# Optimization experiments

Measured on AMD Instinct MI355X. Metric: run time of the kernel, lower is better.

## Reference

```python
import jax, jax.numpy as jnp
import numpy as np

H = W = 64
ALPHA = 1.0
BETA = 100.0
LIMB_PAIRS = np.array([[0,1],[1,2],[2,3],[0,4],[4,5],[5,6],[0,7],[7,8],[8,9],[9,10],
                       [8,11],[11,12],[12,13],[8,14],[14,15],[15,16]])
P0 = LIMB_PAIRS[:, 0]
P1 = LIMB_PAIRS[:, 1]
_last = {}
for _l, _j in enumerate(P0):
    _last[int(_j)] = _l
J0 = np.array(list(_last.keys()))   # unique proximal joints
L0 = np.array(list(_last.values())) # last limb writing to each joint


def make_kernel(h, w, alpha):
    # replicates: coords = stack(meshgrid(arange(2h-1), arange(2w-1))).transpose(1,2) (h==w)
    ii, jj = jnp.meshgrid(jnp.arange(2 * h - 1), jnp.arange(2 * w - 1), indexing='ij')
    ker = jnp.stack([h - jj, w - ii], axis=0).astype(jnp.float32)  # (2, 2h-1, 2w-1)
    dist = jnp.linalg.norm(ker, axis=0, keepdims=True)
    dist = dist.at[0, h, w].set(1.0)
    return ker / dist ** (1.0 + alpha)


def corr_full(x, k):
    # x: (N, Cin, h, w); k: (Cout, Cin, 2h-1, 2w-1); 'same' correlation with pad h-1/w-1
    h, w = x.shape[-2:]
    return jax.lax.conv_general_dilated(x, k, (1, 1), ((h - 1, h - 1), (w - 1, w - 1)))


def heatmap_std(x, di=False):
    axes = (3, 4, 5) if di else (3, 4)
    return jnp.std(x, axis=axes, keepdims=True, ddof=1)


def heatmap_normalize(x, std, di=False):
    return x * std / (heatmap_std(x, di) + 1e-6)


def l2norm(v, axis):
    return v / jnp.maximum(jnp.linalg.norm(v, axis=axis, keepdims=True), 1e-12)


def soft_argmax(hm, beta):
    # hm: ... x h x w -> ... x 2 with (row_coord, col_coord) as in the torch code
    h, w = hm.shape[-2:]
    p = jax.nn.softmax(hm.reshape(hm.shape[:-2] + (-1,)) * beta, axis=-1).reshape(hm.shape)
    rows = jnp.arange(h, dtype=p.dtype)[:, None]
    cols = jnp.arange(w, dtype=p.dtype)[None, :]
    norm = p.sum((-2, -1))
    kp_x = (p * rows).sum((-2, -1)) / norm
    kp_y = (p * cols).sum((-2, -1)) / norm
    return jnp.stack((kp_x, kp_y), axis=-1)


def scale_pts(pts, image_shape, h, w):
    return jnp.stack((pts[..., 0] * image_shape[1] / w,
                      pts[..., 1] * image_shape[0] / h), axis=-1)


def cofix_forward(heatmaps, fields, Ps, Rs, Cs, image_shape, confs, vth1, vth2, pth1, pth2):
    bs, nv, nL, _, h, w = fields.shape
    nJ = heatmaps.shape[2]
    K = make_kernel(h, w, ALPHA)  # (2, 2h-1, 2w-1)

    heatmaps = heatmaps - jnp.mean(heatmaps, axis=(3, 4), keepdims=True)
    std_hm = heatmap_std(heatmaps, di=False)
    std_df = heatmap_std(fields, di=True)

    Hs = heatmaps[:, :, P1] - heatmaps[:, :, P0]  # (bs, nv, nL, h, w)
    # conv3d(kernel1, flipped Hs) == 'same' correlation of Hs with spatially-reversed K
    k1 = K[:, ::-1, ::-1][:, None]  # (2, 1, 2h-1, 2w-1)
    convs = corr_full(Hs.reshape(-1, 1, h, w), k1).reshape(bs, nv, nL, 2, h, w)

    coef = jax.nn.relu(jnp.sum(convs * fields[..., :2, :, :], axis=3, keepdims=True))
    fields_new = fields * coef

    fnorm = jnp.linalg.norm(fields, axis=3, keepdims=True)
    lvecs = l2norm(jnp.sum(fnorm * fields, axis=(4, 5)), axis=3)
    lpts = scale_pts(soft_argmax(fnorm[:, :, :, 0], BETA), image_shape, h, w)

    fnorm_new = jnp.linalg.norm(fields_new, axis=3, keepdims=True)
    lvecs_new = l2norm(jnp.sum(fnorm_new * fields_new, axis=(4, 5)), axis=3)
    lpts_new = scale_pts(soft_argmax(fnorm_new[:, :, :, 0], BETA), image_shape, h, w)

    # original code computes vec_selection(...) then overwrites: delta[:] = 0
    delta = jnp.zeros((bs, nv, nL, 1), dtype=heatmaps.dtype)
    comb_v = delta * lvecs_new + (1 - delta) * lvecs
    comb_p = delta * lpts_new + (1 - delta) * lpts

    d6 = delta[..., None, None]
    fields_c = heatmap_normalize(fields * (1 - d6) + fields_new * d6, std_df, di=True)

    # conv2d(kernel2, fields) then output spatial flip == 'same' correlation with K
    k2 = K[None]  # (1, 2, 2h-1, 2w-1)
    fds2jts = corr_full(fields_c[..., :2, :, :].reshape(-1, 2, h, w), k2)
    fds2jts = fds2jts.reshape(bs, nv, nL, h, w)
    prox_ = jax.nn.relu(-fds2jts)
    dist_ = jax.nn.relu(fds2jts)

    hms_new = heatmaps.at[:, :, J0].set(heatmaps[:, :, J0] * prox_[:, :, L0])
    hms_new = hms_new.at[:, :, P1].set(hms_new[:, :, P1] * dist_)
    hms_new = heatmap_normalize(hms_new, std_hm, di=False)

    kps = scale_pts(soft_argmax(heatmaps, BETA), image_shape, h, w)[..., None]
    kps_new = scale_pts(soft_argmax(hms_new, BETA), image_shape, h, w)[..., None]
    kps_new = jnp.where(jnp.isnan(kps_new), kps, kps_new)

    # sed_selection (reconstructed): keep refined kps where joint conf is high and
    # the refinement displacement is small.
    confs_j = confs[:, :, nL:]
    disp = jnp.linalg.norm((kps_new - kps)[..., 0], axis=-1)  # (bs, nv, nJ)
    sel = ((confs_j > pth1) & (disp < pth2)).astype(kps.dtype)[..., None, None]
    kps_combined = sel * kps_new + (1 - sel) * kps

    return kps_combined, comb_v, comb_p, fields_new, hms_new


def setup_inputs() -> dict:
    key = jax.random.key(0)
    ks = jax.random.split(key, 6)
    bs, nv, nJ, nL = 4, 4, 17, 16
    return {
        'heatmaps': jax.random.uniform(ks[0], (bs, nv, nJ, H, W), jnp.float32),
        'fields': jax.random.normal(ks[1], (bs, nv, nL, 3, H, W), jnp.float32),
        'Ps': jax.random.normal(ks[2], (bs, nv, 3, 4), jnp.float32),
        'Rs': jax.random.normal(ks[3], (bs, nv, 3, 3), jnp.float32),
        'Cs': jax.random.normal(ks[4], (bs, nv, 3, 1), jnp.float32),
        'image_shape': jnp.array([384, 384], jnp.int32),
        'confs': jax.random.uniform(ks[5], (bs, nv, nL + nJ), jnp.float32),
        'vth1': 0.5, 'vth2': 0.5, 'pth1': 0.1, 'pth2': 20.0,
    }


def reference(heatmaps, fields, Ps, Rs, Cs, image_shape, confs, vth1, vth2, pth1, pth2):
    return cofix_forward(heatmaps, fields, Ps, Rs, Cs, image_shape, confs,
                         vth1, vth2, pth1, pth2)
```

## Files before the change

### kernel.cpp

```cpp
#include <hip/hip_runtime.h>
#include <math.h>

#define TPB 1024
#define HTPB 256
#define NPIX 4096
#define NJ 17
#define NL 16
static constexpr float kBeta = 100.0f;
static constexpr float S2H = 0.70710678118654752f;

#define O_KPS 0
#define O_CV 544
#define O_CP 1312
#define O_FN 1824
#define O_HM 3147552
#define W_FDS 0
#define W_MEAN 1048576
#define W_STD 1048848
#define W_SF 1049120
#define W_W1 1049376
#define W_W2 1082144

__device__ __constant__ int c_P0[16] = {0,1,2,0,4,5,0,7,8,9,8,11,12,8,14,15};
__device__ __constant__ int c_P1[16] = {1,2,3,4,5,6,7,8,9,10,11,12,13,14,15,16};
__device__ __constant__ int c_proxL[17] = {6,1,2,-1,4,5,-1,7,13,9,-1,11,12,-1,14,15,-1};
__device__ __constant__ int c_distL[17] = {-1,0,1,2,3,4,5,6,7,8,9,10,11,12,13,14,15};

using cplx = float2;
__device__ inline cplx cadd(cplx a, cplx b){ return {a.x+b.x, a.y+b.y}; }
__device__ inline cplx csub(cplx a, cplx b){ return {a.x-b.x, a.y-b.y}; }
__device__ inline cplx cmul(cplx a, cplx w){ return {a.x*w.x - a.y*w.y, a.x*w.y + a.y*w.x}; }
__device__ inline cplx cmulc(cplx a, cplx w){ return {a.x*w.x + a.y*w.y, a.y*w.x - a.x*w.y}; }

__device__ __constant__ float2 W128BR[8] = {
  {1.f,0.f},
  {0.98078528040323044913f,-0.19509032201612826785f},
  {0.99518472667219688624f,-0.09801714032956060199f},
  {0.95694033573220886494f,-0.29028467725446236764f},
  {0.99879545620517239271f,-0.04906767432741801425f},
  {0.97003125319454399260f,-0.24298017990326388995f},
  {0.98917650996478097345f,-0.14673047445536175166f},
  {0.94154406518302077841f,-0.33688985339222005069f}
};
__device__ __constant__ float2 W16BR[8] = {
  {1.f,0.f},
  {0.f,-1.f},
  {0.70710678118654752440f,-0.70710678118654752440f},
  {-0.70710678118654752440f,-0.70710678118654752440f},
  {0.92387953251128675613f,-0.38268343236508977173f},
  {-0.38268343236508977173f,-0.92387953251128675613f},
  {0.38268343236508977173f,-0.92387953251128675613f},
  {-0.92387953251128675613f,-0.38268343236508977173f}
};

__device__ inline void bf8_tail(cplx t0, cplx t1, cplx t2, cplx t3,
                                cplx t4, cplx t5, cplx t6, cplx t7, cplx x[8]){
  cplx u0=cadd(t0,t2), u2=csub(t0,t2);
  cplx u1=cadd(t1,t3), d13=csub(t1,t3);
  cplx u3={d13.y,-d13.x};
  cplx u4=cadd(t4,t6), u6=csub(t4,t6);
  cplx u5=cadd(t5,t7), d57=csub(t5,t7);
  cplx u7={d57.y,-d57.x};
  x[0]=cadd(u0,u1); x[1]=csub(u0,u1);
  x[2]=cadd(u2,u3); x[3]=csub(u2,u3);
  x[4]=cadd(u4,u5); x[5]=csub(u4,u5);
  x[6]=cadd(u6,u7); x[7]=csub(u6,u7);
}
__device__ inline void bf8_fwd(cplx x[8]){
  cplx t0=cadd(x[0],x[4]), d4=csub(x[0],x[4]);
  cplx t1=cadd(x[1],x[5]), d5=csub(x[1],x[5]);
  cplx t2=cadd(x[2],x[6]), d6=csub(x[2],x[6]);
  cplx t3=cadd(x[3],x[7]), d7=csub(x[3],x[7]);
  cplx t5={S2H*(d5.x+d5.y), S2H*(d5.y-d5.x)};
  cplx t6={d6.y,-d6.x};
  cplx t7={S2H*(d7.y-d7.x), -S2H*(d7.x+d7.y)};
  bf8_tail(t0,t1,t2,t3,d4,t5,t6,t7,x);
}
__device__ inline void bf8_fwd_z(cplx x[8]){
  cplx t5={S2H*(x[1].x+x[1].y), S2H*(x[1].y-x[1].x)};
  cplx t6={x[2].y,-x[2].x};
  cplx t7={S2H*(x[3].y-x[3].x), -S2H*(x[3].x+x[3].y)};
  bf8_tail(x[0],x[1],x[2],x[3],x[0],t5,t6,t7,x);
}
__device__ inline void bf8_inv(cplx y[8]){
  cplx u0=cadd(y[0],y[1]), u1=csub(y[0],y[1]);
  cplx u2=cadd(y[2],y[3]), u3=csub(y[2],y[3]);
  cplx u4=cadd(y[4],y[5]), u5=csub(y[4],y[5]);
  cplx u6=cadd(y[6],y[7]), u7=csub(y[6],y[7]);
  cplx t0=cadd(u0,u2), t2=csub(u0,u2);
  cplx iu3={-u3.y,u3.x};
  cplx t1=cadd(u1,iu3), t3=csub(u1,iu3);
  cplx t4=cadd(u4,u6), t6=csub(u4,u6);
  cplx iu7={-u7.y,u7.x};
  cplx t5=cadd(u5,iu7), t7=csub(u5,iu7);
  y[0]=cadd(t0,t4); y[4]=csub(t0,t4);
  cplx w5={S2H*(t5.x-t5.y), S2H*(t5.x+t5.y)};
  y[1]=cadd(t1,w5); y[5]=csub(t1,w5);
  cplx w6={-t6.y,t6.x};
  y[2]=cadd(t2,w6); y[6]=csub(t2,w6);
  cplx w7={-S2H*(t7.x+t7.y), S2H*(t7.x-t7.y)};
  y[3]=cadd(t3,w7); y[7]=csub(t3,w7);
}

__device__ inline void fft16_fwd(cplx z[16]){
  cplx e[8], o[8];
  #pragma unroll
  for (int t=0;t<8;t++){ e[t]=z[2*t]; o[t]=z[2*t+1]; }
  bf8_fwd(e); bf8_fwd(o);
  #pragma unroll
  for (int p=0;p<8;p++){
    cplx vo = cmul(o[p], W16BR[p]);
    z[2*p]   = cadd(e[p], vo);
    z[2*p+1] = csub(e[p], vo);
  }
}
__device__ inline void fft16_inv(cplx z[16]){
  cplx e[8], o[8];
  #pragma unroll
  for (int p=0;p<8;p++){
    cplx a=z[2*p], b=z[2*p+1];
    e[p] = cadd(a,b);
    o[p] = cmulc(csub(a,b), W16BR[p]);
  }
  bf8_inv(e); bf8_inv(o);
  #pragma unroll
  for (int t=0;t<8;t++){ z[2*t]=e[t]; z[2*t+1]=o[t]; }
}

__device__ inline void twchainA(const cplx* TW, int j, cplx A[8]){
  cplx W1 = TW[j];
  cplx W2 = cmul(W1,W1);
  cplx W4 = cmul(W2,W2);
  cplx W6 = cmul(W4,W2);
  A[0] = {1.f,0.f}; A[1] = W4; A[2] = W2; A[3] = W6;
  A[4] = W1; A[5] = cmul(W4,W1); A[6] = cmul(W2,W1); A[7] = cmul(W6,W1);
}

__device__ inline int PH(int y, int m){ return (y<<6) | ((m ^ ((y&7)*9)) & 63); }

template<int NLINES, bool ZT>
__device__ void row_s1_fwd(float4* S4, const cplx* TW, int tid){
  if (tid < NLINES*8){
    const int L = tid>>3, m = tid&7;
    cplx xe[8], xo[8];
    #pragma unroll
    for (int t=0; t<(ZT?4:8); t++){
      float4 v = S4[PH(L, m+8*t)];
      xe[t]={v.x,v.y}; xo[t]={v.z,v.w};
    }
    if (ZT){ bf8_fwd_z(xe); bf8_fwd_z(xo); } else { bf8_fwd(xe); bf8_fwd(xo); }
    cplx A[8]; twchainA(TW, 2*m, A);
    #pragma unroll
    for (int p=0;p<8;p++){
      cplx B = cmul(A[p], W128BR[p]);
      cplx ve = cmul(xe[p], A[p]);
      cplx vo = cmul(xo[p], B);
      S4[PH(L, m+8*p)] = {ve.x, ve.y, vo.x, vo.y};
    }
  }
  __syncthreads();
}
__device__ void row_s1_fwd64a(float4* S4, const cplx* TW, int tid){
  float2* Sc = (float2*)S4;
  const int u = tid >> 1, ch = tid & 1;
  const int L = u >> 3, m = u & 7;
  cplx x[8];
  #pragma unroll
  for (int t=0;t<4;t++) x[t] = Sc[2*PH(L, m+8*t) + ch];
  bf8_fwd_z(x);
  cplx A[8]; twchainA(TW, 2*m, A);
  #pragma unroll
  for (int p=0;p<8;p++){
    const cplx w = ch ? cmul(A[p], W128BR[p]) : A[p];
    Sc[2*PH(L, m+8*p) + ch] = cmul(x[p], w);
  }
  __syncthreads();
}
__device__ void row_s1_inv64a(float4* S4, const cplx* TW, int tid){
  float2* Sc = (float2*)S4;
  const int u = tid >> 1, ch = tid & 1;
  const int L = u >> 3, m = u & 7;
  cplx x[8];
  #pragma unroll
  for (int p=0;p<8;p++) x[p] = Sc[2*PH(L, m+8*p) + ch];
  cplx A[8]; twchainA(TW, 2*m, A);
  #pragma unroll
  for (int p=0;p<8;p++){
    const cplx w = ch ? cmul(A[p], W128BR[p]) : A[p];
    x[p] = cmulc(x[p], w);
  }
  bf8_inv(x);
  #pragma unroll
  for (int t=0;t<4;t++) Sc[2*PH(L, m+8*t) + ch] = x[t];
  __syncthreads();
}
template<int NLINES>
__device__ void row_s2_fwd(float4* S4, int tid){
  if (tid < NLINES*8){
    const int L = tid>>3, jb = tid&7;
    cplx z[16];
    #pragma unroll
    for (int k=0;k<8;k++){
      float4 v = S4[PH(L, jb*8+k)];
      z[2*k]={v.x,v.y}; z[2*k+1]={v.z,v.w};
    }
    fft16_fwd(z);
    #pragma unroll
    for (int k=0;k<8;k++)
      S4[PH(L, jb*8+k)] = {z[2*k].x, z[2*k].y, z[2*k+1].x, z[2*k+1].y};
  }
  __syncthreads();
}
__device__ void row_s2_inv(float4* S4, int tid){
  if (tid < 512){
    const int L = tid>>3, jb = tid&7;
    cplx z[16];
    #pragma unroll
    for (int k=0;k<8;k++){
      float4 v = S4[PH(L, jb*8+k)];
      z[2*k]={v.x,v.y}; z[2*k+1]={v.z,v.w};
    }
    fft16_inv(z);
    #pragma unroll
    for (int k=0;k<8;k++)
      S4[PH(L, jb*8+k)] = {z[2*k].x, z[2*k].y, z[2*k+1].x, z[2*k+1].y};
  }
  __syncthreads();
}
template<bool ZT>
__device__ void col_s1_fwd(float4* S4, const cplx* TW, int tid){
  const int cp = tid & 63, yj = tid >> 6;
  const int sl = (cp ^ ((yj&7)*9)) & 63;
  cplx xe[8], xo[8];
  #pragma unroll
  for (int t=0; t<(ZT?4:8); t++){
    float4 v = S4[((yj+16*t)<<6) | sl];
    xe[t]={v.x,v.y}; xo[t]={v.z,v.w};
  }
  if (ZT){ bf8_fwd_z(xe); bf8_fwd_z(xo); } else { bf8_fwd(xe); bf8_fwd(xo); }
  cplx A[8]; twchainA(TW, yj, A);
  #pragma unroll
  for (int p=0;p<8;p++){
    cplx ve = cmul(xe[p], A[p]);
    cplx vo = cmul(xo[p], A[p]);
    S4[((yj+16*p)<<6) | sl] = {ve.x, ve.y, vo.x, vo.y};
  }
  __syncthreads();
}
__device__ void col_s1_inv(float4* S4, const cplx* TW, int tid){
  const int cp = tid & 63, yj = tid >> 6;
  const int sl = (cp ^ ((yj&7)*9)) & 63;
  cplx xe[8], xo[8];
  #pragma unroll
  for (int p=0;p<8;p++){
    float4 v = S4[((yj+16*p)<<6) | sl];
    xe[p]={v.x,v.y}; xo[p]={v.z,v.w};
  }
  cplx A[8]; twchainA(TW, yj, A);
  #pragma unroll
  for (int p=0;p<8;p++){
    xe[p] = cmulc(xe[p], A[p]);
    xo[p] = cmulc(xo[p], A[p]);
  }
  bf8_inv(xe); bf8_inv(xo);
  #pragma unroll
  for (int t=0;t<4;t++)
    S4[((yj+16*t)<<6) | sl] = {xe[t].x, xe[t].y, xo[t].x, xo[t].y};
  __syncthreads();
}
__device__ void col_s2_fused(float4* S4, const cplx* __restrict__ Wg, int tid){
  cplx* Sc = (cplx*)S4;
  const int c = tid & 127, r = tid >> 7;
  const int ch = c & 1, cp = c >> 1;
  int ad[16];
  cplx z[16], wv[16];
  #pragma unroll
  for (int i=0;i<16;i++) wv[i] = Wg[(16*r+i)*128 + c];
  #pragma unroll
  for (int i=0;i<16;i++){
    const int y = 16*r + i;
    ad[i] = ((((y<<6) | ((cp ^ ((y&7)*9)) & 63)) << 1) | ch);
    z[i] = Sc[ad[i]];
  }
  fft16_fwd(z);
  #pragma unroll
  for (int i=0;i<16;i++) z[i] = cmul(z[i], wv[i]);
  fft16_inv(z);
  #pragma unroll
  for (int i=0;i<16;i++) Sc[ad[i]] = z[i];
  __syncthreads();
}
__device__ void col_s2_fwd_store(float4* S4, cplx* __restrict__ Wo, int tid){
  cplx* Sc = (cplx*)S4;
  const int c = tid & 127, r = tid >> 7;
  const int ch = c & 1, cp = c >> 1;
  cplx z[16];
  #pragma unroll
  for (int i=0;i<16;i++){
    const int y = 16*r + i;
    z[i] = Sc[(((y<<6) | ((cp ^ ((y&7)*9)) & 63)) << 1) | ch];
  }
  fft16_fwd(z);
  const float scl = 1.0f / 16384.0f;
  #pragma unroll
  for (int i=0;i<16;i++) Wo[(16*r+i)*128 + c] = {z[i].x*scl, z[i].y*scl};
}

__device__ inline float wred(float v){
  #pragma unroll
  for (int o=32;o;o>>=1) v += __shfl_xor(v, o, 64);
  return v;
}
__device__ inline float wredmax(float v){
  #pragma unroll
  for (int o=32;o;o>>=1) v = fmaxf(v, __shfl_xor(v, o, 64));
  return v;
}
template<int NW>
__device__ inline void bred3(float& a, float& b, float& c,
                             float* s0, float* s1, float* s2, int tid){
  a = wred(a); b = wred(b); c = wred(c);
  const int w = tid >> 6;
  if ((tid & 63) == 0){ s0[w]=a; s1[w]=b; s2[w]=c; }
  __syncthreads();
  if (tid == 0){
    float A=0.f, B=0.f, C=0.f;
    #pragma unroll
    for (int i=0;i<NW;i++){ A+=s0[i]; B+=s1[i]; C+=s2[i]; }
    s0[0]=A; s1[0]=B; s2[0]=C;
  }
  __syncthreads();
  a = s0[0]; b = s1[0]; c = s2[0];
  __syncthreads();
}
template<int NW>
__device__ inline float bredmax(float v, float* s0, int tid){
  v = wredmax(v);
  const int w = tid >> 6;
  if ((tid & 63) == 0) s0[w] = v;
  __syncthreads();
  if (tid == 0){
    float M = s0[0];
    #pragma unroll
    for (int i=1;i<NW;i++) M = fmaxf(M, s0[i]);
    s0[0] = M;
  }
  __syncthreads();
  const float r = s0[0];
  __syncthreads();
  return r;
}

__device__ inline cplx wval(int r, int c, int which){
  const int dy = (r<64)? r : r-128;
  const int dx = (c<64)? c : c-128;
  float a, b;
  if (which==0){ a = 1.f-(float)dy; b = 1.f-(float)dx; }
  else         { a = 1.f+(float)dy; b = 1.f+(float)dx; }
  const float den = a*a + b*b;
  if (r==64 || c==64 || den<=0.f) return {0.f,0.f};
  const float inv = 1.f/den;
  return {a*inv, -b*inv};
}

__global__ __launch_bounds__(TPB,4) void pre_kernel(const float* __restrict__ heat,
                                                    const float* __restrict__ fields,
                                                    const int* __restrict__ ishape,
                                                    float* __restrict__ mean_hm,
                                                    float* __restrict__ std_hm,
                                                    float* __restrict__ sf,
                                                    float* __restrict__ W1,
                                                    float* __restrict__ W2,
                                                    float* __restrict__ out){
  __shared__ float4 S4[8192];
  __shared__ cplx TW[128];
  __shared__ float sA[16], sB[16], sC[16];
  const int tid = threadIdx.x;
  const int blk = blockIdx.x;
  if (blk < 2){
    const int which = blk;
    if (tid < 128){
      float s, c;
      sincosf(-6.283185307179586f * (float)tid / 128.0f, &s, &c);
      TW[tid] = {c, s};
    }
    for (int s = tid; s < 8192; s += TPB){
      const int y = s>>6, m = s&63;
      const cplx v0 = wval(y, 2*m, which);
      const cplx v1 = wval(y, 2*m+1, which);
      S4[PH(y, m)] = {v0.x, v0.y, v1.x, v1.y};
    }
    __syncthreads();
    row_s1_fwd<128,false>(S4, TW, tid);
    row_s2_fwd<128>(S4, tid);
    col_s1_fwd<false>(S4, TW, tid);
    col_s2_fwd_store(S4, (cplx*)((which==0)?W1:W2), tid);
  } else if (blk < 274){
    const int n = blk - 2;
    const float* p = heat + (size_t)n * NPIX;
    float s = 0.0f, s2 = 0.0f, d = 0.0f;
    #pragma unroll
    for (int i = 0; i < 4; i++){
      const float x = p[tid + i*TPB];
      s += x; s2 += x*x;
    }
    bred3<16>(s, s2, d, sA, sB, sC, tid);
    if (tid == 0){
      const float mean = s / 4096.0f;
      const float var = (s2 - s*mean) / 4095.0f;
      mean_hm[n] = mean;
      std_hm[n] = sqrtf(fmaxf(var, 0.0f));
    }
  } else {
    const int m = blk - 274;
    const float* f = fields + (size_t)m * 3 * NPIX;
    float s1 = 0.0f, s2 = 0.0f;
    float a0 = 0.0f, a1 = 0.0f, a2 = 0.0f;
    float fn[4];
    #pragma unroll
    for (int i = 0; i < 4; i++){
      const int px = tid + i*TPB;
      const float f0 = f[px], f1 = f[NPIX+px], f2 = f[2*NPIX+px];
      s1 += f0+f1+f2; s2 += f0*f0+f1*f1+f2*f2;
      const float nn = sqrtf(f0*f0 + f1*f1 + f2*f2);
      fn[i] = nn;
      a0 += nn*f0; a1 += nn*f1; a2 += nn*f2;
    }
    {
      float t1 = s1, t2 = s2, t3 = 0.0f;
      bred3<16>(t1, t2, t3, sA, sB, sC, tid);
      if (tid == 0){
        const float var = (t2 - t1*t1/12288.0f) / 12287.0f;
        const float sd = sqrtf(fmaxf(var, 0.0f));
        sf[m] = sd / (sd + 1e-6f);
      }
    }
    bred3<16>(a0, a1, a2, sA, sB, sC, tid);
    float mx = fmaxf(fmaxf(fn[0],fn[1]), fmaxf(fn[2],fn[3]));
    mx = bredmax<16>(mx, sA, tid);
    float Sm = 0.0f, Sx = 0.0f, Sy = 0.0f;
    #pragma unroll
    for (int i = 0; i < 4; i++){
      const int px = tid + i*TPB;
      const float e = expf(kBeta * (fn[i] - mx));
      Sm += e; Sx += e * (float)(px>>6); Sy += e * (float)(px&63);
    }
    bred3<16>(Sm, Sx, Sy, sA, sB, sC, tid);
    if (tid == 0){
      float nrm = sqrtf(a0*a0 + a1*a1 + a2*a2);
      nrm = fmaxf(nrm, 1e-12f);
      out[O_CV + m*3 + 0] = a0/nrm;
      out[O_CV + m*3 + 1] = a1/nrm;
      out[O_CV + m*3 + 2] = a2/nrm;
      const float sxs = (float)ishape[1] / 64.0f;
      const float sys = (float)ishape[0] / 64.0f;
      out[O_CP + m*2 + 0] = Sx/Sm * sxs;
      out[O_CP + m*2 + 1] = Sy/Sm * sys;
    }
  }
}

__global__ __launch_bounds__(TPB,4) void conv_kernel(const float* __restrict__ heat,
                                                     const float* __restrict__ mean_hm,
                                                     const float* __restrict__ fields,
                                                     const float* __restrict__ sf,
                                                     const float* __restrict__ W1g,
                                                     const float* __restrict__ W2g,
                                                     float* __restrict__ out_fn,
                                                     float* __restrict__ fds){
  __shared__ float4 S4[8192];
  __shared__ cplx TW[128];
  const int tid = threadIdx.x;
  const int n = blockIdx.x;
  const bool is2 = (n < 256);
  const int m_img = is2 ? n : (n - 256);
  if (tid < 128){
    float s, c;
    sincosf(-6.283185307179586f * (float)tid / 128.0f, &s, &c);
    TW[tid] = {c, s};
  }
  const float* f = fields + (size_t)m_img * 3 * NPIX;
  if (!is2){
    const int bv = m_img >> 4, l = m_img & 15;
    const int j1 = bv*NJ + c_P1[l], j0 = bv*NJ + c_P0[l];
    const float* h1 = heat + (size_t)j1 * NPIX;
    const float* h0 = heat + (size_t)j0 * NPIX;
    const float dm = mean_hm[j1] - mean_hm[j0];
    for (int s = tid; s < 2048; s += TPB){
      const int y = s>>5, m = s&31;
      const int i = (y<<6) + 2*m;
      const float2 a = *(const float2*)(h1 + i);
      const float2 b = *(const float2*)(h0 + i);
      S4[PH(y, m)] = {a.x - b.x - dm, 0.f, a.y - b.y - dm, 0.f};
    }
  } else {
    for (int s = tid; s < 2048; s += TPB){
      const int y = s>>5, m = s&31;
      const int i = (y<<6) + 2*m;
      const float2 a = *(const float2*)(f + NPIX + i);
      const float2 b = *(const float2*)(f + i);
      S4[PH(y, m)] = {a.x, b.x, a.y, b.y};
    }
  }
  __syncthreads();
  row_s1_fwd64a(S4, TW, tid);
  row_s2_fwd<64>(S4, tid);
  col_s1_fwd<true>(S4, TW, tid);
  col_s2_fused(S4, (const cplx*)(is2 ? W2g : W1g), tid);
  col_s1_inv(S4, TW, tid);
  row_s2_inv(S4, tid);
  row_s1_inv64a(S4, TW, tid);
  if (!is2){
    float* o = out_fn + (size_t)m_img * 3 * NPIX;
    for (int s = tid; s < 2048; s += TPB){
      const int y = s>>5, m = s&31;
      const int i = (y<<6) + 2*m;
      const float4 v = S4[PH(y, m)];
      const float2 f0 = *(const float2*)(f + i);
      const float2 f1 = *(const float2*)(f + NPIX + i);
      const float2 f2 = *(const float2*)(f + 2*NPIX + i);
      const float cA = fmaxf(0.f, (-v.y)*f0.x + v.x*f1.x);
      const float cB = fmaxf(0.f, (-v.w)*f0.y + v.z*f1.y);
      *(float2*)(o + i)          = {f0.x*cA, f0.y*cB};
      *(float2*)(o + NPIX + i)   = {f1.x*cA, f1.y*cB};
      *(float2*)(o + 2*NPIX + i) = {f2.x*cA, f2.y*cB};
    }
  } else {
    const float sc = sf[m_img];
    float* o = fds + (size_t)m_img * NPIX;
    for (int s = tid; s < 2048; s += TPB){
      const int y = s>>5, m = s&31;
      const int i = (y<<6) + 2*m;
      const float4 v = S4[PH(y, m)];
      *(float2*)(o + i) = {v.x*sc, v.z*sc};
    }
  }
}

__global__ __launch_bounds__(HTPB) void hms_kernel(const float* __restrict__ heat,
                                                   const float* __restrict__ mean_hm,
                                                   const float* __restrict__ std_hm,
                                                   const float* __restrict__ fds,
                                                   const float* __restrict__ confs,
                                                   const int* __restrict__ ishape,
                                                   const float* __restrict__ pth1p,
                                                   const float* __restrict__ pth2p,
                                                   float* __restrict__ out){
  __shared__ float sA[4], sB[4], sC[4];
  const int tid = threadIdx.x;
  const int idx = blockIdx.x;
  const int bv = idx / NJ, j = idx % NJ;
  const float* hp = heat + (size_t)idx * NPIX;
  const float mh = mean_hm[idx];
  const int pl = c_proxL[j], dl = c_distL[j];
  const float* fp = (pl >= 0) ? fds + (size_t)(bv*NL + pl) * NPIX : nullptr;
  const float* fd = (dl >= 0) ? fds + (size_t)(bv*NL + dl) * NPIX : nullptr;
  float ho[16], hn[16];
  float s = 0.0f, s2 = 0.0f, dummy = 0.0f;
  #pragma unroll
  for (int i = 0; i < 16; i++){
    const int px = tid + i*HTPB;
    const float h = hp[px] - mh;
    ho[i] = h;
    float m = h;
    if (pl >= 0) m *= fmaxf(0.0f, -fp[px]);
    if (dl >= 0) m *= fmaxf(0.0f, fd[px]);
    hn[i] = m;
    s += m; s2 += m*m;
  }
  bred3<4>(s, s2, dummy, sA, sB, sC, tid);
  const float var = (s2 - s*s/4096.0f) / 4095.0f;
  const float sdn = sqrtf(fmaxf(var, 0.0f));
  const float scale = std_hm[idx] / (sdn + 1e-6f);
  float* ohm = out + O_HM + (size_t)idx * NPIX;
  #pragma unroll
  for (int i = 0; i < 16; i++){
    hn[i] *= scale;
    ohm[tid + i*HTPB] = hn[i];
  }
  float mo = -1e30f, mn = -1e30f;
  #pragma unroll
  for (int i = 0; i < 16; i++){ mo = fmaxf(mo, ho[i]); mn = fmaxf(mn, hn[i]); }
  mo = bredmax<4>(mo, sA, tid);
  mn = bredmax<4>(mn, sA, tid);
  float So = 0.0f, Sxo = 0.0f, Syo = 0.0f;
  float Sn = 0.0f, Sxn = 0.0f, Syn = 0.0f;
  #pragma unroll
  for (int i = 0; i < 16; i++){
    const int px = tid + i*HTPB;
    const float y = (float)(px >> 6), x = (float)(px & 63);
    const float eo = expf(kBeta * (ho[i] - mo));
    So += eo; Sxo += eo*y; Syo += eo*x;
    const float en = expf(kBeta * (hn[i] - mn));
    Sn += en; Sxn += en*y; Syn += en*x;
  }
  bred3<4>(So, Sxo, Syo, sA, sB, sC, tid);
  bred3<4>(Sn, Sxn, Syn, sA, sB, sC, tid);
  if (tid == 0){
    const float sxs = (float)ishape[1] / 64.0f;
    const float sys = (float)ishape[0] / 64.0f;
    const float kxo = Sxo/So * sxs, kyo = Syo/So * sys;
    float kxn = Sxn/Sn * sxs, kyn = Syn/Sn * sys;
    if (kxn != kxn) kxn = kxo;
    if (kyn != kyn) kyn = kyo;
    const float ddx = kxn - kxo, ddy = kyn - kyo;
    const float disp = sqrtf(ddx*ddx + ddy*ddy);
    const float conf = confs[bv*(NL+NJ) + NL + j];
    const bool sel = (conf > pth1p[0]) && (disp < pth2p[0]);
    out[O_KPS + idx*2 + 0] = sel ? kxn : kxo;
    out[O_KPS + idx*2 + 1] = sel ? kyn : kyo;
  }
}

extern "C" void kernel_launch(void* const* d_in, const int* in_sizes, int n_in,
                              void* d_out, int out_size, void* d_ws, size_t ws_size,
                              hipStream_t stream) {
  const float* heat   = (const float*)d_in[0];
  const float* fields = (const float*)d_in[1];
  const int*   ishape = (const int*)d_in[5];
  const float* confs  = (const float*)d_in[6];
  const float* pth1   = (const float*)d_in[9];
  const float* pth2   = (const float*)d_in[10];
  float* out = (float*)d_out;
  float* ws = (float*)d_ws;
  float* fds     = ws + W_FDS;
  float* mean_hm = ws + W_MEAN;
  float* std_hm  = ws + W_STD;
  float* sf      = ws + W_SF;
  float* W1      = ws + W_W1;
  float* W2      = ws + W_W2;

  hipLaunchKernelGGL(pre_kernel, dim3(530), dim3(TPB), 0, stream,
                     heat, fields, ishape, mean_hm, std_hm, sf, W1, W2, out);
  hipLaunchKernelGGL(conv_kernel, dim3(512), dim3(TPB), 0, stream,
                     heat, mean_hm, fields, sf, W1, W2, out + O_FN, fds);
  hipLaunchKernelGGL(hms_kernel, dim3(272), dim3(HTPB), 0, stream,
                     heat, mean_hm, std_hm, fds, confs, ishape, pth1, pth2, out);
}
```

Before: 153.0 us.

## Assign FFT stages to waves, replace block barriers with wave-local LDS waits, vectorize loads

Reassigns the FFT work so that consecutive row stages and consecutive column stages are each handled within a single wavefront. This lets most block-wide __syncthreads calls become an s_waitcnt on LDS, meant to cut barrier stalls across the forward and inverse 2D FFT passes. It also changes the LDS swizzle to add an extra XOR term, and widens the global loads and stores in the stats, FFT and heatmap kernels to float4. Correctness depends on each wave touching only the data it wrote between the wave-local waits, and the new thread mapping halves the active threads in the row stages.

```diff
diff --git a/kernel.cpp b/kernel.cpp
--- a/kernel.cpp
+++ b/kernel.cpp
@@ -31,6 +31,10 @@
 __device__ inline cplx csub(cplx a, cplx b){ return {a.x-b.x, a.y-b.y}; }
 __device__ inline cplx cmul(cplx a, cplx w){ return {a.x*w.x - a.y*w.y, a.x*w.y + a.y*w.x}; }
 __device__ inline cplx cmulc(cplx a, cplx w){ return {a.x*w.x + a.y*w.y, a.y*w.x - a.x*w.y}; }
+
+__device__ inline void wsync(){
+  asm volatile("s_waitcnt lgkmcnt(0)" ::: "memory");
+}
 
 __device__ __constant__ float2 W128BR[8] = {
   {1.f,0.f},
@@ -136,105 +140,77 @@
   A[4] = W1; A[5] = cmul(W4,W1); A[6] = cmul(W2,W1); A[7] = cmul(W6,W1);
 }
 
-__device__ inline int PH(int y, int m){ return (y<<6) | ((m ^ ((y&7)*9)) & 63); }
-
-template<int NLINES, bool ZT>
-__device__ void row_s1_fwd(float4* S4, const cplx* TW, int tid){
-  if (tid < NLINES*8){
-    const int L = tid>>3, m = tid&7;
-    cplx xe[8], xo[8];
-    #pragma unroll
-    for (int t=0; t<(ZT?4:8); t++){
-      float4 v = S4[PH(L, m+8*t)];
-      xe[t]={v.x,v.y}; xo[t]={v.z,v.w};
-    }
-    if (ZT){ bf8_fwd_z(xe); bf8_fwd_z(xo); } else { bf8_fwd(xe); bf8_fwd(xo); }
-    cplx A[8]; twchainA(TW, 2*m, A);
-    #pragma unroll
-    for (int p=0;p<8;p++){
-      cplx B = cmul(A[p], W128BR[p]);
-      cplx ve = cmul(xe[p], A[p]);
-      cplx vo = cmul(xo[p], B);
-      S4[PH(L, m+8*p)] = {ve.x, ve.y, vo.x, vo.y};
-    }
-  }
-  __syncthreads();
-}
-__device__ void row_s1_fwd64a(float4* S4, const cplx* TW, int tid){
-  float2* Sc = (float2*)S4;
-  const int u = tid >> 1, ch = tid & 1;
-  const int L = u >> 3, m = u & 7;
-  cplx x[8];
-  #pragma unroll
-  for (int t=0;t<4;t++) x[t] = Sc[2*PH(L, m+8*t) + ch];
-  bf8_fwd_z(x);
+__device__ inline int PH(int y, int m){
+  return (y<<6) | ((m ^ ((y&7)*9) ^ ((y>>3)&7)) & 63);
+}
+
+template<bool ZT>
+__device__ inline void row_s1_f(float4* S4, const cplx* TW, int L, int m){
+  cplx xe[8], xo[8];
+  #pragma unroll
+  for (int t=0; t<(ZT?4:8); t++){
+    float4 v = S4[PH(L, m+8*t)];
+    xe[t]={v.x,v.y}; xo[t]={v.z,v.w};
+  }
+  if (ZT){ bf8_fwd_z(xe); bf8_fwd_z(xo); } else { bf8_fwd(xe); bf8_fwd(xo); }
   cplx A[8]; twchainA(TW, 2*m, A);
   #pragma unroll
   for (int p=0;p<8;p++){
-    const cplx w = ch ? cmul(A[p], W128BR[p]) : A[p];
-    Sc[2*PH(L, m+8*p) + ch] = cmul(x[p], w);
-  }
-  __syncthreads();
-}
-__device__ void row_s1_inv64a(float4* S4, const cplx* TW, int tid){
-  float2* Sc = (float2*)S4;
-  const int u = tid >> 1, ch = tid & 1;
-  const int L = u >> 3, m = u & 7;
-  cplx x[8];
-  #pragma unroll
-  for (int p=0;p<8;p++) x[p] = Sc[2*PH(L, m+8*p) + ch];
+    cplx B = cmul(A[p], W128BR[p]);
+    cplx ve = cmul(xe[p], A[p]);
+    cplx vo = cmul(xo[p], B);
+    S4[PH(L, m+8*p)] = {ve.x, ve.y, vo.x, vo.y};
+  }
+}
+__device__ inline void row_s1_i(float4* S4, const cplx* TW, int L, int m){
+  cplx xe[8], xo[8];
+  #pragma unroll
+  for (int p=0;p<8;p++){
+    float4 v = S4[PH(L, m+8*p)];
+    xe[p]={v.x,v.y}; xo[p]={v.z,v.w};
+  }
   cplx A[8]; twchainA(TW, 2*m, A);
   #pragma unroll
   for (int p=0;p<8;p++){
-    const cplx w = ch ? cmul(A[p], W128BR[p]) : A[p];
-    x[p] = cmulc(x[p], w);
-  }
-  bf8_inv(x);
-  #pragma unroll
-  for (int t=0;t<4;t++) Sc[2*PH(L, m+8*t) + ch] = x[t];
-  __syncthreads();
-}
-template<int NLINES>
-__device__ void row_s2_fwd(float4* S4, int tid){
-  if (tid < NLINES*8){
-    const int L = tid>>3, jb = tid&7;
-    cplx z[16];
-    #pragma unroll
-    for (int k=0;k<8;k++){
-      float4 v = S4[PH(L, jb*8+k)];
-      z[2*k]={v.x,v.y}; z[2*k+1]={v.z,v.w};
-    }
-    fft16_fwd(z);
-    #pragma unroll
-    for (int k=0;k<8;k++)
-      S4[PH(L, jb*8+k)] = {z[2*k].x, z[2*k].y, z[2*k+1].x, z[2*k+1].y};
-  }
-  __syncthreads();
-}
-__device__ void row_s2_inv(float4* S4, int tid){
-  if (tid < 512){
-    const int L = tid>>3, jb = tid&7;
-    cplx z[16];
-    #pragma unroll
-    for (int k=0;k<8;k++){
-      float4 v = S4[PH(L, jb*8+k)];
-      z[2*k]={v.x,v.y}; z[2*k+1]={v.z,v.w};
-    }
-    fft16_inv(z);
-    #pragma unroll
-    for (int k=0;k<8;k++)
-      S4[PH(L, jb*8+k)] = {z[2*k].x, z[2*k].y, z[2*k+1].x, z[2*k+1].y};
-  }
-  __syncthreads();
+    cplx B = cmul(A[p], W128BR[p]);
+    xe[p] = cmulc(xe[p], A[p]);
+    xo[p] = cmulc(xo[p], B);
+  }
+  bf8_inv(xe); bf8_inv(xo);
+  #pragma unroll
+  for (int t=0;t<4;t++)
+    S4[PH(L, m+8*t)] = {xe[t].x, xe[t].y, xo[t].x, xo[t].y};
+}
+__device__ inline void row_s2_f(float4* S4, int L, int jb){
+  cplx z[16];
+  #pragma unroll
+  for (int k=0;k<8;k++){
+    float4 v = S4[PH(L, jb*8+k)];
+    z[2*k]={v.x,v.y}; z[2*k+1]={v.z,v.w};
+  }
+  fft16_fwd(z);
+  #pragma unroll
+  for (int k=0;k<8;k++)
+    S4[PH(L, jb*8+k)] = {z[2*k].x, z[2*k].y, z[2*k+1].x, z[2*k+1].y};
+}
+__device__ inline void row_s2_i(float4* S4, int L, int jb){
+  cplx z[16];
+  #pragma unroll
+  for (int k=0;k<8;k++){
+    float4 v = S4[PH(L, jb*8+k)];
+    z[2*k]={v.x,v.y}; z[2*k+1]={v.z,v.w};
+  }
+  fft16_inv(z);
+  #pragma unroll
+  for (int k=0;k<8;k++)
+    S4[PH(L, jb*8+k)] = {z[2*k].x, z[2*k].y, z[2*k+1].x, z[2*k+1].y};
 }
 template<bool ZT>
-__device__ void col_s1_fwd(float4* S4, const cplx* TW, int tid){
-  const int cp = tid & 63, yj = tid >> 6;
-  const int sl = (cp ^ ((yj&7)*9)) & 63;
+__device__ inline void col_s1_f(float4* S4, const cplx* TW, int yj, int sc){
   cplx xe[8], xo[8];
   #pragma unroll
   for (int t=0; t<(ZT?4:8); t++){
-    float4 v = S4[((yj+16*t)<<6) | sl];
+    float4 v = S4[PH(yj+16*t, sc)];
     xe[t]={v.x,v.y}; xo[t]={v.z,v.w};
   }
   if (ZT){ bf8_fwd_z(xe); bf8_fwd_z(xo); } else { bf8_fwd(xe); bf8_fwd(xo); }
@@ -243,17 +219,14 @@
   for (int p=0;p<8;p++){
     cplx ve = cmul(xe[p], A[p]);
     cplx vo = cmul(xo[p], A[p]);
-    S4[((yj+16*p)<<6) | sl] = {ve.x, ve.y, vo.x, vo.y};
-  }
-  __syncthreads();
-}
-__device__ void col_s1_inv(float4* S4, const cplx* TW, int tid){
-  const int cp = tid & 63, yj = tid >> 6;
-  const int sl = (cp ^ ((yj&7)*9)) & 63;
+    S4[PH(yj+16*p, sc)] = {ve.x, ve.y, vo.x, vo.y};
+  }
+}
+__device__ inline void col_s1_i(float4* S4, const cplx* TW, int yj, int sc){
   cplx xe[8], xo[8];
   #pragma unroll
   for (int p=0;p<8;p++){
-    float4 v = S4[((yj+16*p)<<6) | sl];
+    float4 v = S4[PH(yj+16*p, sc)];
     xe[p]={v.x,v.y}; xo[p]={v.z,v.w};
   }
   cplx A[8]; twchainA(TW, yj, A);
@@ -265,45 +238,7 @@
   bf8_inv(xe); bf8_inv(xo);
   #pragma unroll
   for (int t=0;t<4;t++)
-    S4[((yj+16*t)<<6) | sl] = {xe[t].x, xe[t].y, xo[t].x, xo[t].y};
-  __syncthreads();
-}
-__device__ void col_s2_fused(float4* S4, const cplx* __restrict__ Wg, int tid){
-  cplx* Sc = (cplx*)S4;
-  const int c = tid & 127, r = tid >> 7;
-  const int ch = c & 1, cp = c >> 1;
-  int ad[16];
-  cplx z[16], wv[16];
-  #pragma unroll
-  for (int i=0;i<16;i++) wv[i] = Wg[(16*r+i)*128 + c];
-  #pragma unroll
-  for (int i=0;i<16;i++){
-    const int y = 16*r + i;
-    ad[i] = ((((y<<6) | ((cp ^ ((y&7)*9)) & 63)) << 1) | ch);
-    z[i] = Sc[ad[i]];
-  }
-  fft16_fwd(z);
-  #pragma unroll
-  for (int i=0;i<16;i++) z[i] = cmul(z[i], wv[i]);
-  fft16_inv(z);
-  #pragma unroll
-  for (int i=0;i<16;i++) Sc[ad[i]] = z[i];
-  __syncthreads();
-}
-__device__ void col_s2_fwd_store(float4* S4, cplx* __restrict__ Wo, int tid){
-  cplx* Sc = (cplx*)S4;
-  const int c = tid & 127, r = tid >> 7;
-  const int ch = c & 1, cp = c >> 1;
-  cplx z[16];
-  #pragma unroll
-  for (int i=0;i<16;i++){
-    const int y = 16*r + i;
-    z[i] = Sc[(((y<<6) | ((cp ^ ((y&7)*9)) & 63)) << 1) | ch];
-  }
-  fft16_fwd(z);
-  const float scl = 1.0f / 16384.0f;
-  #pragma unroll
-  for (int i=0;i<16;i++) Wo[(16*r+i)*128 + c] = {z[i].x*scl, z[i].y*scl};
+    S4[PH(yj+16*t, sc)] = {xe[t].x, xe[t].y, xo[t].x, xo[t].y};
 }
 
 __device__ inline float wred(float v){
@@ -376,6 +311,7 @@
   __shared__ cplx TW[128];
   __shared__ float sA[16], sB[16], sC[16];
   const int tid = threadIdx.x;
+  const int wv = tid >> 6, lane = tid & 63;
   const int blk = blockIdx.x;
   if (blk < 2){
     const int which = blk;
@@ -391,19 +327,36 @@
       S4[PH(y, m)] = {v0.x, v0.y, v1.x, v1.y};
     }
     __syncthreads();
-    row_s1_fwd<128,false>(S4, TW, tid);
-    row_s2_fwd<128>(S4, tid);
-    col_s1_fwd<false>(S4, TW, tid);
-    col_s2_fwd_store(S4, (cplx*)((which==0)?W1:W2), tid);
+    {
+      const int L = 8*wv + (lane>>3), m = lane&7;
+      row_s1_f<false>(S4, TW, L, m);
+      wsync();
+      row_s2_f(S4, L, m);
+    }
+    __syncthreads();
+    {
+      const int yj = lane & 15, sc = 4*wv + (lane>>4);
+      col_s1_f<false>(S4, TW, yj, sc);
+      wsync();
+      cplx* Sc = (cplx*)S4;
+      const int c = 8*wv + (lane&7), r = lane>>3;
+      cplx z[16];
+      #pragma unroll
+      for (int i=0;i<16;i++)
+        z[i] = Sc[2*PH(16*r+i, c>>1) + (c&1)];
+      fft16_fwd(z);
+      cplx* Wo = (cplx*)((which==0)?W1:W2);
+      const float scl = 1.0f / 16384.0f;
+      #pragma unroll
+      for (int i=0;i<16;i++) Wo[(16*r+i)*128 + c] = {z[i].x*scl, z[i].y*scl};
+    }
   } else if (blk < 274){
     const int n = blk - 2;
-    const float* p = heat + (size_t)n * NPIX;
-    float s = 0.0f, s2 = 0.0f, d = 0.0f;
-    #pragma unroll
-    for (int i = 0; i < 4; i++){
-      const float x = p[tid + i*TPB];
-      s += x; s2 += x*x;
-    }
+    const float4* p4 = (const float4*)(heat + (size_t)n * NPIX);
+    const float4 x = p4[tid];
+    float s = x.x+x.y+x.z+x.w;
+    float s2 = x.x*x.x + x.y*x.y + x.z*x.z + x.w*x.w;
+    float d = 0.0f;
     bred3<16>(s, s2, d, sA, sB, sC, tid);
     if (tid == 0){
       const float mean = s / 4096.0f;
@@ -413,18 +366,21 @@
     }
   } else {
     const int m = blk - 274;
-    const float* f = fields + (size_t)m * 3 * NPIX;
+    const float4* F4 = (const float4*)(fields + (size_t)m * 3 * NPIX);
+    const float4 f0 = F4[tid], f1 = F4[1024+tid], f2 = F4[2048+tid];
+    const float f0a[4] = {f0.x,f0.y,f0.z,f0.w};
+    const float f1a[4] = {f1.x,f1.y,f1.z,f1.w};
+    const float f2a[4] = {f2.x,f2.y,f2.z,f2.w};
+    float fn[4];
     float s1 = 0.0f, s2 = 0.0f;
     float a0 = 0.0f, a1 = 0.0f, a2 = 0.0f;
-    float fn[4];
     #pragma unroll
-    for (int i = 0; i < 4; i++){
-      const int px = tid + i*TPB;
-      const float f0 = f[px], f1 = f[NPIX+px], f2 = f[2*NPIX+px];
-      s1 += f0+f1+f2; s2 += f0*f0+f1*f1+f2*f2;
-      const float nn = sqrtf(f0*f0 + f1*f1 + f2*f2);
-      fn[i] = nn;
-      a0 += nn*f0; a1 += nn*f1; a2 += nn*f2;
+    for (int j = 0; j < 4; j++){
+      s1 += f0a[j]+f1a[j]+f2a[j];
+      s2 += f0a[j]*f0a[j]+f1a[j]*f1a[j]+f2a[j]*f2a[j];
+      const float nn = sqrtf(f0a[j]*f0a[j] + f1a[j]*f1a[j] + f2a[j]*f2a[j]);
+      fn[j] = nn;
+      a0 += nn*f0a[j]; a1 += nn*f1a[j]; a2 += nn*f2a[j];
     }
     {
       float t1 = s1, t2 = s2, t3 = 0.0f;
@@ -440,9 +396,9 @@
     mx = bredmax<16>(mx, sA, tid);
     float Sm = 0.0f, Sx = 0.0f, Sy = 0.0f;
     #pragma unroll
-    for (int i = 0; i < 4; i++){
-      const int px = tid + i*TPB;
-      const float e = expf(kBeta * (fn[i] - mx));
+    for (int j = 0; j < 4; j++){
+      const int px = tid*4 + j;
+      const float e = expf(kBeta * (fn[j] - mx));
       Sm += e; Sx += e * (float)(px>>6); Sy += e * (float)(px&63);
     }
     bred3<16>(Sm, Sx, Sy, sA, sB, sC, tid);
@@ -471,6 +427,7 @@
   __shared__ float4 S4[8192];
   __shared__ cplx TW[128];
   const int tid = threadIdx.x;
+  const int wv = tid >> 6, lane = tid & 63;
   const int n = blockIdx.x;
   const bool is2 = (n < 256);
   const int m_img = is2 ? n : (n - 256);
@@ -480,59 +437,98 @@
     TW[tid] = {c, s};
   }
   const float* f = fields + (size_t)m_img * 3 * NPIX;
-  if (!is2){
-    const int bv = m_img >> 4, l = m_img & 15;
-    const int j1 = bv*NJ + c_P1[l], j0 = bv*NJ + c_P0[l];
-    const float* h1 = heat + (size_t)j1 * NPIX;
-    const float* h0 = heat + (size_t)j0 * NPIX;
-    const float dm = mean_hm[j1] - mean_hm[j0];
-    for (int s = tid; s < 2048; s += TPB){
-      const int y = s>>5, m = s&31;
-      const int i = (y<<6) + 2*m;
-      const float2 a = *(const float2*)(h1 + i);
-      const float2 b = *(const float2*)(h0 + i);
-      S4[PH(y, m)] = {a.x - b.x - dm, 0.f, a.y - b.y - dm, 0.f};
-    }
-  } else {
-    for (int s = tid; s < 2048; s += TPB){
-      const int y = s>>5, m = s&31;
-      const int i = (y<<6) + 2*m;
-      const float2 a = *(const float2*)(f + NPIX + i);
-      const float2 b = *(const float2*)(f + i);
-      S4[PH(y, m)] = {a.x, b.x, a.y, b.y};
-    }
-  }
-  __syncthreads();
-  row_s1_fwd64a(S4, TW, tid);
-  row_s2_fwd<64>(S4, tid);
-  col_s1_fwd<true>(S4, TW, tid);
-  col_s2_fused(S4, (const cplx*)(is2 ? W2g : W1g), tid);
-  col_s1_inv(S4, TW, tid);
-  row_s2_inv(S4, tid);
-  row_s1_inv64a(S4, TW, tid);
-  if (!is2){
-    float* o = out_fn + (size_t)m_img * 3 * NPIX;
-    for (int s = tid; s < 2048; s += TPB){
-      const int y = s>>5, m = s&31;
-      const int i = (y<<6) + 2*m;
-      const float4 v = S4[PH(y, m)];
-      const float2 f0 = *(const float2*)(f + i);
-      const float2 f1 = *(const float2*)(f + NPIX + i);
-      const float2 f2 = *(const float2*)(f + 2*NPIX + i);
-      const float cA = fmaxf(0.f, (-v.y)*f0.x + v.x*f1.x);
-      const float cB = fmaxf(0.f, (-v.w)*f0.y + v.z*f1.y);
-      *(float2*)(o + i)          = {f0.x*cA, f0.y*cB};
-      *(float2*)(o + NPIX + i)   = {f1.x*cA, f1.y*cB};
-      *(float2*)(o + 2*NPIX + i) = {f2.x*cA, f2.y*cB};
-    }
-  } else {
-    const float sc = sf[m_img];
-    float* o = fds + (size_t)m_img * NPIX;
-    for (int s = tid; s < 2048; s += TPB){
-      const int y = s>>5, m = s&31;
-      const int i = (y<<6) + 2*m;
-      const float4 v = S4[PH(y, m)];
-      *(float2*)(o + i) = {v.x*sc, v.z*sc};
+  {
+    const int y = tid >> 4, x4 = (tid & 15) << 2;
+    const int i = (y << 6) + x4;
+    const int m = (tid & 15) << 1;
+    if (!is2){
+      const int bv = m_img >> 4, l = m_img & 15;
+      const int j1 = bv*NJ + c_P1[l], j0 = bv*NJ + c_P0[l];
+      const float dm = mean_hm[j1] - mean_hm[j0];
+      const float4 a = *(const float4*)(heat + (size_t)j1*NPIX + i);
+      const float4 b = *(const float4*)(heat + (size_t)j0*NPIX + i);
+      S4[PH(y, m  )] = {a.x-b.x-dm, 0.f, a.y-b.y-dm, 0.f};
+      S4[PH(y, m+1)] = {a.z-b.z-dm, 0.f, a.w-b.w-dm, 0.f};
+    } else {
+      const float4 A = *(const float4*)(f + NPIX + i);
+      const float4 B = *(const float4*)(f + i);
+      S4[PH(y, m  )] = {A.x, B.x, A.y, B.y};
+      S4[PH(y, m+1)] = {A.z, B.z, A.w, B.w};
+    }
+  }
+  __syncthreads();
+  if (wv < 8){
+    const int L = 8*wv + (lane>>3), m = lane&7;
+    row_s1_f<true>(S4, TW, L, m);
+    wsync();
+    row_s2_f(S4, L, m);
+  }
+  __syncthreads();
+  {
+    const cplx* Wg = (const cplx*)(is2 ? W2g : W1g);
+    const int c = 8*wv + (lane&7), r = lane>>3;
+    cplx wvv[16];
+    #pragma unroll
+    for (int i=0;i<16;i++) wvv[i] = Wg[(16*r+i)*128 + c];
+    const int yj = lane & 15, sc = 4*wv + (lane>>4);
+    col_s1_f<true>(S4, TW, yj, sc);
+    wsync();
+    {
+      cplx* Sc = (cplx*)S4;
+      cplx z[16];
+      int ad[16];
+      #pragma unroll
+      for (int i=0;i<16;i++){
+        ad[i] = 2*PH(16*r+i, c>>1) + (c&1);
+        z[i] = Sc[ad[i]];
+      }
+      fft16_fwd(z);
+      #pragma unroll
+      for (int i=0;i<16;i++) z[i] = cmul(z[i], wvv[i]);
+      fft16_inv(z);
+      #pragma unroll
+      for (int i=0;i<16;i++) Sc[ad[i]] = z[i];
+    }
+    wsync();
+    col_s1_i(S4, TW, yj, sc);
+  }
+  __syncthreads();
+  if (wv < 8){
+    const int L = 8*wv + (lane>>3), m = lane&7;
+    row_s2_i(S4, L, m);
+    wsync();
+    row_s1_i(S4, TW, L, m);
+  }
+  __syncthreads();
+  {
+    const int y = tid >> 4, x4 = (tid & 15) << 2;
+    const int i = (y << 6) + x4;
+    const int m = (tid & 15) << 1;
+    const float4 va = S4[PH(y, m)];
+    const float4 vb = S4[PH(y, m+1)];
+    if (!is2){
+      float* o = out_fn + (size_t)m_img * 3 * NPIX;
+      const float4 f0 = *(const float4*)(f + i);
+      const float4 f1 = *(const float4*)(f + NPIX + i);
+      const float4 f2 = *(const float4*)(f + 2*NPIX + i);
+      const float c0[4] = {-va.y, -va.w, -vb.y, -vb.w};
+      const float c1[4] = { va.x,  va.z,  vb.x,  vb.z};
+      const float f0a[4] = {f0.x,f0.y,f0.z,f0.w};
+      const float f1a[4] = {f1.x,f1.y,f1.z,f1.w};
+      const float f2a[4] = {f2.x,f2.y,f2.z,f2.w};
+      float o0[4], o1[4], o2[4];
+      #pragma unroll
+      for (int j=0;j<4;j++){
+        const float cf = fmaxf(0.f, c0[j]*f0a[j] + c1[j]*f1a[j]);
+        o0[j] = f0a[j]*cf; o1[j] = f1a[j]*cf; o2[j] = f2a[j]*cf;
+      }
+      *(float4*)(o + i)          = {o0[0],o0[1],o0[2],o0[3]};
+      *(float4*)(o + NPIX + i)   = {o1[0],o1[1],o1[2],o1[3]};
+      *(float4*)(o + 2*NPIX + i) = {o2[0],o2[1],o2[2],o2[3]};
+    } else {
+      const float sc2 = sf[m_img];
+      float* o = fds + (size_t)m_img * NPIX;
+      *(float4*)(o + i) = {va.x*sc2, va.z*sc2, vb.x*sc2, vb.z*sc2};
     }
   }
 }
@@ -550,33 +546,48 @@
   const int tid = threadIdx.x;
   const int idx = blockIdx.x;
   const int bv = idx / NJ, j = idx % NJ;
-  const float* hp = heat + (size_t)idx * NPIX;
+  const float4* hp4 = (const float4*)(heat + (size_t)idx * NPIX);
   const float mh = mean_hm[idx];
   const int pl = c_proxL[j], dl = c_distL[j];
-  const float* fp = (pl >= 0) ? fds + (size_t)(bv*NL + pl) * NPIX : nullptr;
-  const float* fd = (dl >= 0) ? fds + (size_t)(bv*NL + dl) * NPIX : nullptr;
+  const float4* fp4 = (pl >= 0) ? (const float4*)(fds + (size_t)(bv*NL + pl) * NPIX) : nullptr;
+  const float4* fd4 = (dl >= 0) ? (const float4*)(fds + (size_t)(bv*NL + dl) * NPIX) : nullptr;
   float ho[16], hn[16];
   float s = 0.0f, s2 = 0.0f, dummy = 0.0f;
   #pragma unroll
-  for (int i = 0; i < 16; i++){
-    const int px = tid + i*HTPB;
-    const float h = hp[px] - mh;
-    ho[i] = h;
-    float m = h;
-    if (pl >= 0) m *= fmaxf(0.0f, -fp[px]);
-    if (dl >= 0) m *= fmaxf(0.0f, fd[px]);
-    hn[i] = m;
-    s += m; s2 += m*m;
+  for (int i = 0; i < 4; i++){
+    const int u = tid + i*HTPB;
+    const float4 h4 = hp4[u];
+    const float hv[4] = {h4.x-mh, h4.y-mh, h4.z-mh, h4.w-mh};
+    float pv[4] = {1.f,1.f,1.f,1.f};
+    if (pl >= 0){
+      const float4 p4 = fp4[u];
+      pv[0] = fmaxf(0.f,-p4.x); pv[1] = fmaxf(0.f,-p4.y);
+      pv[2] = fmaxf(0.f,-p4.z); pv[3] = fmaxf(0.f,-p4.w);
+    }
+    float dv[4] = {1.f,1.f,1.f,1.f};
+    if (dl >= 0){
+      const float4 d4 = fd4[u];
+      dv[0] = fmaxf(0.f,d4.x); dv[1] = fmaxf(0.f,d4.y);
+      dv[2] = fmaxf(0.f,d4.z); dv[3] = fmaxf(0.f,d4.w);
+    }
+    #pragma unroll
+    for (int k=0;k<4;k++){
+      ho[4*i+k] = hv[k];
+      const float m = hv[k]*pv[k]*dv[k];
+      hn[4*i+k] = m;
+      s += m; s2 += m*m;
+    }
   }
   bred3<4>(s, s2, dummy, sA, sB, sC, tid);
   const float var = (s2 - s*s/4096.0f) / 4095.0f;
   const float sdn = sqrtf(fmaxf(var, 0.0f));
   const float scale = std_hm[idx] / (sdn + 1e-6f);
-  float* ohm = out + O_HM + (size_t)idx * NPIX;
-  #pragma unroll
-  for (int i = 0; i < 16; i++){
-    hn[i] *= scale;
-    ohm[tid + i*HTPB] = hn[i];
+  float4* ohm4 = (float4*)(out + O_HM + (size_t)idx * NPIX);
+  #pragma unroll
+  for (int i = 0; i < 4; i++){
+    #pragma unroll
+    for (int k=0;k<4;k++) hn[4*i+k] *= scale;
+    ohm4[tid + i*HTPB] = {hn[4*i], hn[4*i+1], hn[4*i+2], hn[4*i+3]};
   }
   float mo = -1e30f, mn = -1e30f;
   #pragma unroll
@@ -587,7 +598,7 @@
   float Sn = 0.0f, Sxn = 0.0f, Syn = 0.0f;
   #pragma unroll
   for (int i = 0; i < 16; i++){
-    const int px = tid + i*HTPB;
+    const int px = (tid + (i>>2)*HTPB)*4 + (i&3);
     const float y = (float)(px >> 6), x = (float)(px & 63);
     const float eo = expf(kBeta * (ho[i] - mo));
     So += eo; Sxo += eo*y; Syo += eo*x;
```

Measured after the change: 142.8 us. 6.6% less time.
